# Kernel optimization log

Hardware: AMD Instinct MI355X
Metric: run time of the kernel (lower is better)

## Reference

```python
import jax, jax.numpy as jnp
import numpy as np
from jax import lax

B_, L_, C_IN = 32, 1024, 3
D_MODEL, D_STATE, D_CONV, EXPAND = 256, 16, 4, 2
D_INNER = EXPAND * D_MODEL           # 512
DT_RANK = D_MODEL // 16              # 16
N_HEADS, N_CLASS = 8, 10
LN_EPS = 1e-5


def _pos_emb(L, d):
    pos = np.arange(L, dtype=np.float32)[:, None]
    div = np.exp(np.arange(0, d, 2, dtype=np.float32) * (-np.log(10000.0) / d))
    pe = np.zeros((L, d), np.float32)
    pe[:, 0::2] = np.sin(pos * div)
    pe[:, 1::2] = np.cos(pos * div)
    return jnp.asarray(pe)


def setup_inputs() -> dict:
    key = jax.random.key(0)
    ks = jax.random.split(key, 12)
    f = lambda k, shp, s: jax.random.normal(k, shp, jnp.float32) * s
    return {
        'x_enc': f(ks[0], (B_, L_, C_IN), 1.0),
        'x_mark_enc': jnp.ones((B_, L_), jnp.float32),
        'conv_emb_w': f(ks[1], (D_MODEL, C_IN, 3), (2.0 / (C_IN * 3)) ** 0.5),
        'in_proj_w': f(ks[2], (2 * D_INNER, D_MODEL), D_MODEL ** -0.5),
        'conv1d_w': f(ks[3], (D_INNER, 1, D_CONV), D_CONV ** -0.5),
        'conv1d_b': f(ks[4], (D_INNER,), 0.02),
        'x_proj_w': f(ks[5], (DT_RANK + 2 * D_STATE, D_INNER), D_INNER ** -0.5),
        'dt_proj_w': f(ks[6], (D_INNER, DT_RANK), DT_RANK ** -0.5),
        'dt_proj_b': f(ks[7], (D_INNER,), 0.1) - 2.0,
        'A_log': jnp.log(jnp.tile(jnp.arange(1, D_STATE + 1, dtype=jnp.float32), (D_INNER, 1))),
        'D': jnp.ones((D_INNER,), jnp.float32),
        'out_proj_w': f(ks[8], (D_MODEL, D_INNER), D_INNER ** -0.5),
        'ln_g': jnp.ones((D_MODEL,), jnp.float32),
        'ln_b': jnp.zeros((D_MODEL,), jnp.float32),
        'out_w': f(ks[9], (N_CLASS, D_MODEL), D_MODEL ** -0.5),
        'attn_w': f(ks[10], (N_HEADS, D_MODEL), 0.02),
        'attn_b': jnp.ones((N_HEADS,), jnp.float32),
    }


def _forward(x_enc, x_mark_enc, conv_emb_w, in_proj_w, conv1d_w, conv1d_b,
             x_proj_w, dt_proj_w, dt_proj_b, A_log, D, out_proj_w,
             ln_g, ln_b, out_w, attn_w, attn_b):
    silu = jax.nn.silu
    # --- embedding: Conv1d 'same' with replicate padding + sinusoidal PE ---
    xp = jnp.pad(x_enc, ((0, 0), (1, 1), (0, 0)), mode='edge')      # k=3 -> pad (1,1)
    x = lax.conv_general_dilated(xp.transpose(0, 2, 1), conv_emb_w, (1,), 'VALID',
                                 dimension_numbers=('NCH', 'OIH', 'NCH')).transpose(0, 2, 1)
    x = x + _pos_emb(L_, D_MODEL)[None]                              # (B,L,D)

    # --- Mamba_TimeVariant (standard Mamba selective scan) ---
    xz = jnp.einsum('bld,ed->ble', x, in_proj_w)                     # (B,L,2*Din)
    xin, z = xz[..., :D_INNER], xz[..., D_INNER:]
    # depthwise causal conv, kernel D_CONV
    xc = jnp.pad(xin.transpose(0, 2, 1), ((0, 0), (0, 0), (D_CONV - 1, 0)))
    xc = lax.conv_general_dilated(xc, conv1d_w, (1,), 'VALID',
                                  feature_group_count=D_INNER,
                                  dimension_numbers=('NCH', 'OIH', 'NCH'))
    xc = silu(xc.transpose(0, 2, 1) + conv1d_b)                      # (B,L,Din)

    dbl = jnp.einsum('bld,ed->ble', xc, x_proj_w)                    # (B,L,dt_rank+2*N)
    dtr = dbl[..., :DT_RANK]
    Bm = dbl[..., DT_RANK:DT_RANK + D_STATE]                         # (B,L,N)
    Cm = dbl[..., DT_RANK + D_STATE:]                                # (B,L,N)
    dt = jax.nn.softplus(jnp.einsum('blr,dr->bld', dtr, dt_proj_w) + dt_proj_b)
    A = -jnp.exp(A_log)                                              # (Din,N)

    def step(h, inp):
        dt_t, B_t, C_t, x_t = inp                                    # (B,Din),(B,N),(B,N),(B,Din)
        dA = jnp.exp(dt_t[..., None] * A)                            # (B,Din,N)
        h = dA * h + dt_t[..., None] * B_t[:, None, :] * x_t[..., None]
        y = jnp.einsum('bdn,bn->bd', h, C_t)
        return h, y

    h0 = jnp.zeros((B_, D_INNER, D_STATE), xc.dtype)
    inputs = (dt.transpose(1, 0, 2), Bm.transpose(1, 0, 2),
              Cm.transpose(1, 0, 2), xc.transpose(1, 0, 2))
    _, ys = lax.scan(step, h0, inputs)                               # (L,B,Din)
    y = ys.transpose(1, 0, 2) + xc * D                               # skip via D
    y = y * silu(z)
    m = jnp.einsum('bld,ed->ble', y, out_proj_w)                     # (B,L,Dmodel)

    # LayerNorm + SiLU
    mu = m.mean(-1, keepdims=True)
    var = ((m - mu) ** 2).mean(-1, keepdims=True)
    m = (m - mu) * lax.rsqrt(var + LN_EPS) * ln_g + ln_b
    m = silu(m)

    # classification head
    logit = jnp.einsum('bld,cd->blc', m, out_w) * x_mark_enc[..., None]
    s = jnp.einsum('bld,hd->blh', m, attn_w) + attn_b                # (B,L,H)
    w = jax.nn.softmax(jnp.max(s, axis=2, keepdims=True), axis=1)    # (B,L,1)
    return (logit * w).sum(1)                                        # (B,num_class)


def reference(x_enc, x_mark_enc, conv_emb_w, in_proj_w, conv1d_w, conv1d_b,
              x_proj_w, dt_proj_w, dt_proj_b, A_log, D, out_proj_w,
              ln_g, ln_b, out_w, attn_w, attn_b):
    return _forward(x_enc, x_mark_enc, conv_emb_w, in_proj_w, conv1d_w, conv1d_b,
                    x_proj_w, dt_proj_w, dt_proj_b, A_log, D, out_proj_w,
                    ln_g, ln_b, out_w, attn_w, attn_b)
```

## Files before the change

### kernel.cpp

```cpp
#include <hip/hip_runtime.h>
#include <hip/hip_bf16.h>
#include <math.h>

#define B_  32
#define L_  1024
#define CIN 3
#define DM  256
#define DI  512
#define NST 16
#define NH  8
#define NC  10
#define M_TOT (B_*L_)

typedef unsigned short u16;
typedef __attribute__((ext_vector_type(8))) short bf16x8;
typedef __attribute__((ext_vector_type(4))) float f32x4;

static __device__ __forceinline__ float sigmoidf_(float x) {
    return 1.0f / (1.0f + __expf(-x));
}
static __device__ __forceinline__ u16 f2bf(float f) {
    unsigned int u = __float_as_uint(f);
    return (u16)((u + 0x7FFF + ((u >> 16) & 1)) >> 16);
}
static __device__ __forceinline__ float bf2f(u16 u) {
    return __uint_as_float(((unsigned int)u) << 16);
}

static __device__ __forceinline__ void reduce16_pair(float& a, float& b) {
    asm volatile(
        "s_nop 1\n\t"
        "v_add_f32 %0, %0, %0 quad_perm:[1,0,3,2] row_mask:0xf bank_mask:0xf\n\t"
        "v_add_f32 %1, %1, %1 quad_perm:[1,0,3,2] row_mask:0xf bank_mask:0xf\n\t"
        "s_nop 1\n\t"
        "v_add_f32 %0, %0, %0 quad_perm:[2,3,0,1] row_mask:0xf bank_mask:0xf\n\t"
        "v_add_f32 %1, %1, %1 quad_perm:[2,3,0,1] row_mask:0xf bank_mask:0xf\n\t"
        "s_nop 1\n\t"
        "v_add_f32 %0, %0, %0 row_ror:4 row_mask:0xf bank_mask:0xf\n\t"
        "v_add_f32 %1, %1, %1 row_ror:4 row_mask:0xf bank_mask:0xf\n\t"
        "s_nop 1\n\t"
        "v_add_f32 %0, %0, %0 row_ror:8 row_mask:0xf bank_mask:0xf\n\t"
        "v_add_f32 %1, %1, %1 row_ror:8 row_mask:0xf bank_mask:0xf\n\t"
        "s_nop 1\n\t"
        : "+v"(a), "+v"(b));
}

__global__ __launch_bounds__(256) void k_cvt(const float* __restrict__ in,
        u16* __restrict__ out) {
    int i = (blockIdx.x * 256 + threadIdx.x) * 4;
    float4 v = *(const float4*)(in + i);
    ushort4 o;
    o.x = f2bf(v.x); o.y = f2bf(v.y); o.z = f2bf(v.z); o.w = f2bf(v.w);
    *(ushort4*)(out + i) = o;
}

__global__ __launch_bounds__(256) void k_embed(const float* __restrict__ xe,
        const float* __restrict__ w, u16* __restrict__ x) {
    int bl = blockIdx.x;
    int l = bl & (L_-1);
    int b = bl >> 10;
    int d = threadIdx.x;
    const float* xb = xe + (size_t)b * L_ * CIN;
    int t0 = l > 0 ? l-1 : 0;
    int t2 = l < L_-1 ? l+1 : L_-1;
    const float* w3 = w + d*9;
    float acc = 0.f;
    #pragma unroll
    for (int i = 0; i < 3; ++i) {
        acc += xb[t0*3+i] * w3[i*3+0];
        acc += xb[l *3+i] * w3[i*3+1];
        acc += xb[t2*3+i] * w3[i*3+2];
    }
    int j = d >> 1;
    float div = expf((float)(2*j) * (-logf(10000.0f)/(float)DM));
    float ang = (float)l * div;
    acc += (d & 1) ? cosf(ang) : sinf(ang);
    x[(size_t)bl*DM + d] = f2bf(acc);
}

#define GST 40
__global__ __launch_bounds__(256) void k_gemm_mfma(
        const u16* __restrict__ A, const u16* __restrict__ W,
        float* __restrict__ O1, u16* __restrict__ O2b,
        int M, int N, int K, int S) {
    __shared__ u16 As[128*GST];
    __shared__ u16 Bs[128*GST];
    int tid = threadIdx.x;
    int row0 = blockIdx.y * 128, col0 = blockIdx.x * 128;
    int wave = tid >> 6, lane = tid & 63;
    int wr = (wave >> 1) * 64, wc = (wave & 1) * 64;
    int l16 = lane & 15, kl = lane >> 4;
    int srow = tid >> 1, skh = (tid & 1) * 16;
    const u16* Ag = A + (size_t)(row0 + srow) * K + skh;
    const u16* Wg = W + (size_t)(col0 + srow) * K + skh;

    f32x4 acc[4][4];
    #pragma unroll
    for (int m = 0; m < 4; ++m)
        #pragma unroll
        for (int n = 0; n < 4; ++n)
            acc[m][n] = (f32x4){0.f, 0.f, 0.f, 0.f};

    for (int k0 = 0; k0 < K; k0 += 32) {
        uint4 a0 = *(const uint4*)(Ag + k0);
        uint4 a1 = *(const uint4*)(Ag + k0 + 8);
        uint4 b0 = *(const uint4*)(Wg + k0);
        uint4 b1 = *(const uint4*)(Wg + k0 + 8);
        __syncthreads();
        *(uint4*)&As[srow*GST + skh]     = a0;
        *(uint4*)&As[srow*GST + skh + 8] = a1;
        *(uint4*)&Bs[srow*GST + skh]     = b0;
        *(uint4*)&Bs[srow*GST + skh + 8] = b1;
        __syncthreads();
        bf16x8 af[4], bf[4];
        #pragma unroll
        for (int m = 0; m < 4; ++m)
            af[m] = *(const bf16x8*)&As[(wr + m*16 + l16)*GST + kl*8];
        #pragma unroll
        for (int n = 0; n < 4; ++n)
            bf[n] = *(const bf16x8*)&Bs[(wc + n*16 + l16)*GST + kl*8];
        #pragma unroll
        for (int m = 0; m < 4; ++m)
            #pragma unroll
            for (int n = 0; n < 4; ++n)
                acc[m][n] = __builtin_amdgcn_mfma_f32_16x16x32_bf16(
                                af[m], bf[n], acc[m][n], 0, 0, 0);
    }

    #pragma unroll
    for (int m = 0; m < 4; ++m) {
        int rbase = row0 + wr + m*16 + kl*4;
        #pragma unroll
        for (int n = 0; n < 4; ++n) {
            int col = col0 + wc + n*16 + l16;
            #pragma unroll
            for (int r = 0; r < 4; ++r) {
                float v = acc[m][n][r];
                if (col < S) O1[(size_t)(rbase + r)*S + col] = v;
                else         O2b[(size_t)(rbase + r)*(N - S) + (col - S)] = f2bf(v);
            }
        }
    }
}

__global__ __launch_bounds__(256) void k_conv(const float* __restrict__ xin,
        const float* __restrict__ w, const float* __restrict__ bias,
        float* __restrict__ xc) {
    size_t idx = (size_t)blockIdx.x * 256 + threadIdx.x;
    int d = (int)(idx & (DI-1));
    size_t m = idx >> 9;
    int l = (int)(m & (L_-1));
    float acc = bias[d];
    #pragma unroll
    for (int k = 0; k < 4; ++k) {
        int t = l + k - 3;
        if (t >= 0)
            acc = fmaf(xin[idx + ((size_t)(k-3))*DI], w[d*4 + k], acc);
    }
    xc[idx] = acc * sigmoidf_(acc);
}

#define XBM 128
#define XBK 16
__global__ __launch_bounds__(256) void k_xproj(const float* __restrict__ xc,
        const float* __restrict__ wp, float* __restrict__ dbl) {
    __shared__ float As[XBK][XBM];
    __shared__ float Ws[XBK][48];
    int tid = threadIdx.x;
    int row0 = blockIdx.x * XBM;
    int lr = tid >> 1;
    int lk = (tid & 1) * 8;
    int we = tid >> 2;
    int wk = (tid & 3) * 4;
    int tx = tid & 15;
    int ty = tid >> 4;
    float acc[8][3];
    #pragma unroll
    for (int i = 0; i < 8; ++i)
        #pragma unroll
        for (int j = 0; j < 3; ++j) acc[i][j] = 0.f;

    for (int k0 = 0; k0 < DI; k0 += XBK) {
        float4 a0 = *(const float4*)(xc + (size_t)(row0+lr)*DI + k0 + lk);
        float4 a1 = *(const float4*)(xc + (size_t)(row0+lr)*DI + k0 + lk + 4);
        float4 w0 = make_float4(0.f,0.f,0.f,0.f);
        if (tid < 192) w0 = *(const float4*)(wp + (size_t)we*DI + k0 + wk);
        __syncthreads();
        As[lk+0][lr]=a0.x; As[lk+1][lr]=a0.y; As[lk+2][lr]=a0.z; As[lk+3][lr]=a0.w;
        As[lk+4][lr]=a1.x; As[lk+5][lr]=a1.y; As[lk+6][lr]=a1.z; As[lk+7][lr]=a1.w;
        if (tid < 192) {
            Ws[wk+0][we]=w0.x; Ws[wk+1][we]=w0.y; Ws[wk+2][we]=w0.z; Ws[wk+3][we]=w0.w;
        }
        __syncthreads();
        #pragma unroll
        for (int k = 0; k < XBK; ++k) {
            float4 av0 = *(const float4*)&As[k][ty*8];
            float4 av1 = *(const float4*)&As[k][ty*8+4];
            float w0_ = Ws[k][tx*3+0];
            float w1_ = Ws[k][tx*3+1];
            float w2_ = Ws[k][tx*3+2];
            float ar[8] = {av0.x,av0.y,av0.z,av0.w,av1.x,av1.y,av1.z,av1.w};
            #pragma unroll
            for (int i = 0; i < 8; ++i) {
                acc[i][0] = fmaf(ar[i], w0_, acc[i][0]);
                acc[i][1] = fmaf(ar[i], w1_, acc[i][1]);
                acc[i][2] = fmaf(ar[i], w2_, acc[i][2]);
            }
        }
    }
    #pragma unroll
    for (int i = 0; i < 8; ++i) {
        size_t r = row0 + ty*8 + i;
        #pragma unroll
        for (int j = 0; j < 3; ++j)
            dbl[r*48 + tx*3 + j] = acc[i][j];
    }
}

__global__ __launch_bounds__(256) void k_dtproj(const float* __restrict__ dbl,
        const float* __restrict__ dtw, const float* __restrict__ dtb,
        float* __restrict__ dt) {
    __shared__ float wl[DI][17];
    __shared__ float rl[32][16];
    size_t m0 = (size_t)blockIdx.x * 32;
    for (int i = threadIdx.x; i < DI*16; i += 256)
        wl[i >> 4][i & 15] = dtw[i];
    for (int i = threadIdx.x; i < 32*16; i += 256)
        rl[i >> 4][i & 15] = dbl[(m0 + (i>>4))*48 + (i & 15)];
    __syncthreads();
    float b0 = dtb[threadIdx.x];
    float b1 = dtb[256 + threadIdx.x];
    for (int mm = 0; mm < 32; ++mm) {
        #pragma unroll
        for (int half = 0; half < 2; ++half) {
            int d = half*256 + threadIdx.x;
            float acc = half ? b1 : b0;
            #pragma unroll
            for (int r = 0; r < 16; ++r)
                acc = fmaf(rl[mm][r], wl[d][r], acc);
            float sp = fmaxf(acc, 0.f) + log1pf(__expf(-fabsf(acc)));
            dt[(m0+mm)*DI + d] = sp;
        }
    }
}

#define SCAN_T 64
__global__ __launch_bounds__(256) void k_scan(const float* __restrict__ dt,
        const float* __restrict__ xc, const float* __restrict__ dbl,
        const float* __restrict__ A_log, const float* __restrict__ Dp,
        const u16* __restrict__ zbf, u16* __restrict__ ybf) {
    __shared__ float4 sq4[SCAN_T*17];
    __shared__ float2 sBC2[SCAN_T*17];

    int tid = threadIdx.x;
    int ch = tid >> 4;
    int n  = tid & 15;
    int d0 = blockIdx.x * 16;
    int b  = blockIdx.y;
    int d  = d0 + ch;
    float Avl2 = -expf(A_log[(size_t)d*NST + n]) * 1.44269504f;
    float h = 0.f;
    size_t base = (size_t)b * L_;

    int st = tid >> 2;
    int sc = (tid & 3) * 4;
    float4 Dv = *(const float4*)(Dp + d0 + sc);

    for (int t0 = 0; t0 < L_; t0 += SCAN_T) {
        __syncthreads();
        {
            size_t row = base + t0 + st;
            float4 dtv = *(const float4*)(dt + row*DI + d0 + sc);
            float4 xv  = *(const float4*)(xc + row*DI + d0 + sc);
            ushort4 zv4 = *(const ushort4*)(zbf + row*DI + d0 + sc);
            float4 Bv  = *(const float4*)(dbl + row*48 + 16 + sc);
            float4 Cv  = *(const float4*)(dbl + row*48 + 32 + sc);
            float z0 = bf2f(zv4.x), z1 = bf2f(zv4.y);
            float z2 = bf2f(zv4.z), z3 = bf2f(zv4.w);
            float g0 = z0 * sigmoidf_(z0);
            float g1 = z1 * sigmoidf_(z1);
            float g2 = z2 * sigmoidf_(z2);
            float g3 = z3 * sigmoidf_(z3);
            sq4[st*17 + sc+0] = make_float4(dtv.x, dtv.x*xv.x, xv.x*Dv.x*g0, g0);
            sq4[st*17 + sc+1] = make_float4(dtv.y, dtv.y*xv.y, xv.y*Dv.y*g1, g1);
            sq4[st*17 + sc+2] = make_float4(dtv.z, dtv.z*xv.z, xv.z*Dv.z*g2, g2);
            sq4[st*17 + sc+3] = make_float4(dtv.w, dtv.w*xv.w, xv.w*Dv.w*g3, g3);
            sBC2[st*17 + sc+0] = make_float2(Bv.x, Cv.x);
            sBC2[st*17 + sc+1] = make_float2(Bv.y, Cv.y);
            sBC2[st*17 + sc+2] = make_float2(Bv.z, Cv.z);
            sBC2[st*17 + sc+3] = make_float2(Bv.w, Cv.w);
        }
        __syncthreads();

        #pragma unroll 2
        for (int t2 = 0; t2 < SCAN_T/2; ++t2) {
            float2 bc0 = sBC2[(2*t2)*17 + n];
            float2 bc1 = sBC2[(2*t2+1)*17 + n];
            float4 q0 = sq4[(2*t2)*17 + ch];
            float4 q1 = sq4[(2*t2+1)*17 + ch];
            float dA = exp2f(q0.x * Avl2);
            h = fmaf(dA, h, q0.y * bc0.x);
            float p0 = h * bc0.y;
            dA = exp2f(q1.x * Avl2);
            h = fmaf(dA, h, q1.y * bc1.x);
            float p1 = h * bc1.y;
            reduce16_pair(p0, p1);
            if (n == 0) {
                size_t row = base + t0 + 2*t2;
                ybf[row*DI + d]     = f2bf(fmaf(p0, q0.w, q0.z));
                ybf[(row+1)*DI + d] = f2bf(fmaf(p1, q1.w, q1.z));
            }
        }
    }
}

__global__ __launch_bounds__(256) void k_lnsilu(float* __restrict__ m,
        const float* __restrict__ g, const float* __restrict__ bta) {
    size_t row = (size_t)blockIdx.x*4 + (threadIdx.x >> 6);
    int lane = threadIdx.x & 63;
    float4 v = *(const float4*)(m + row*DM + lane*4);
    float s = v.x + v.y + v.z + v.w;
    #pragma unroll
    for (int o = 32; o > 0; o >>= 1) s += __shfl_xor(s, o);
    float mu = s * (1.0f/DM);
    float4 c = make_float4(v.x-mu, v.y-mu, v.z-mu, v.w-mu);
    float s2 = c.x*c.x + c.y*c.y + c.z*c.z + c.w*c.w;
    #pragma unroll
    for (int o = 32; o > 0; o >>= 1) s2 += __shfl_xor(s2, o);
    float rstd = 1.0f / sqrtf(s2 * (1.0f/DM) + 1e-5f);
    float4 gv = *(const float4*)(g + lane*4);
    float4 bv = *(const float4*)(bta + lane*4);
    float o0 = c.x*rstd*gv.x + bv.x;
    float o1 = c.y*rstd*gv.y + bv.y;
    float o2 = c.z*rstd*gv.z + bv.z;
    float o3 = c.w*rstd*gv.w + bv.w;
    float4 r;
    r.x = o0 * sigmoidf_(o0);
    r.y = o1 * sigmoidf_(o1);
    r.z = o2 * sigmoidf_(o2);
    r.w = o3 * sigmoidf_(o3);
    *(float4*)(m + row*DM + lane*4) = r;
}

#define HBK 32
__global__ __launch_bounds__(256) void k_heads18(const float* __restrict__ m,
        const float* __restrict__ aw, const float* __restrict__ ow,
        float* __restrict__ r18) {
    __shared__ float As[128][36];
    __shared__ float Ws[18][36];
    int tid = threadIdx.x;
    int row0 = blockIdx.x * 128;
    int r = tid >> 1, ch = tid & 1, cb = ch * 9;
    int sr = tid >> 1, sk = (tid & 1) * 16;
    float acc[9];
    #pragma unroll
    for (int c = 0; c < 9; ++c) acc[c] = 0.f;

    for (int k0 = 0; k0 < DM; k0 += HBK) {
        float4 a[4];
        #pragma unroll
        for (int q = 0; q < 4; ++q)
            a[q] = *(const float4*)(m + (size_t)(row0+sr)*DM + k0 + sk + q*4);
        float4 wv = make_float4(0.f,0.f,0.f,0.f);
        int wc = tid >> 3, wk = (tid & 7) * 4;
        if (tid < 144) {
            const float* wsrc = (wc < NH) ? (aw + wc*DM) : (ow + (wc-NH)*DM);
            wv = *(const float4*)(wsrc + k0 + wk);
        }
        __syncthreads();
        #pragma unroll
        for (int q = 0; q < 4; ++q)
            *(float4*)&As[sr][sk + q*4] = a[q];
        if (tid < 144)
            *(float4*)&Ws[wc][wk] = wv;
        __syncthreads();
        #pragma unroll
        for (int k4 = 0; k4 < HBK/4; ++k4) {
            float4 av = *(const float4*)&As[r][k4*4];
            #pragma unroll
            for (int c = 0; c < 9; ++c) {
                float4 w4 = *(const float4*)&Ws[cb + c][k4*4];
                acc[c] += av.x*w4.x + av.y*w4.y + av.z*w4.z + av.w*w4.w;
            }
        }
        __syncthreads();
    }
    #pragma unroll
    for (int c = 0; c < 9; ++c)
        r18[(size_t)(row0 + r)*18 + cb + c] = acc[c];
}

__global__ __launch_bounds__(256) void k_final(const float* __restrict__ r18,
        const float* __restrict__ ab, const float* __restrict__ xmark,
        float* __restrict__ out) {
    __shared__ float e[L_];
    __shared__ float red[256];
    int b = blockIdx.x;
    int tid = threadIdx.x;
    float abr[NH];
    #pragma unroll
    for (int j = 0; j < NH; ++j) abr[j] = ab[j];
    float mx = -1e30f;
    for (int l = tid; l < L_; l += 256) {
        const float* rr = r18 + ((size_t)b*L_ + l)*18;
        float sm = rr[0] + abr[0];
        #pragma unroll
        for (int j = 1; j < NH; ++j) sm = fmaxf(sm, rr[j] + abr[j]);
        e[l] = sm;
        mx = fmaxf(mx, sm);
    }
    #pragma unroll
    for (int o = 32; o > 0; o >>= 1) mx = fmaxf(mx, __shfl_xor(mx, o));
    red[tid] = mx;
    __syncthreads();
    mx = fmaxf(fmaxf(red[0], red[64]), fmaxf(red[128], red[192]));
    __syncthreads();
    float ssum = 0.f;
    for (int l = tid; l < L_; l += 256) {
        float ev = __expf(e[l] - mx);
        e[l] = ev;
        ssum += ev;
    }
    #pragma unroll
    for (int o = 32; o > 0; o >>= 1) ssum += __shfl_xor(ssum, o);
    if ((tid & 63) == 0) red[tid >> 6] = ssum;
    __syncthreads();
    float inv = 1.0f / (red[0]+red[1]+red[2]+red[3]);
    float acc[NC];
    #pragma unroll
    for (int c = 0; c < NC; ++c) acc[c] = 0.f;
    for (int l = tid; l < L_; l += 256) {
        float wl = e[l] * xmark[(size_t)b*L_ + l];
        const float* lg = r18 + ((size_t)b*L_ + l)*18 + NH;
        #pragma unroll
        for (int c = 0; c < NC; ++c) acc[c] = fmaf(wl, lg[c], acc[c]);
    }
    __syncthreads();
    for (int c = 0; c < NC; ++c) {
        red[tid] = acc[c];
        __syncthreads();
        if (tid < 64) {
            float s2 = red[tid]+red[tid+64]+red[tid+128]+red[tid+192];
            #pragma unroll
            for (int o = 32; o > 0; o >>= 1) s2 += __shfl_xor(s2, o);
            if (tid == 0) out[(size_t)b*NC + c] = s2 * inv;
        }
        __syncthreads();
    }
}

extern "C" void kernel_launch(void* const* d_in, const int* in_sizes, int n_in,
                              void* d_out, int out_size, void* d_ws, size_t ws_size,
                              hipStream_t stream) {
    const float* x_enc  = (const float*)d_in[0];
    const float* x_mark = (const float*)d_in[1];
    const float* cemb_w = (const float*)d_in[2];
    const float* inp_w  = (const float*)d_in[3];
    const float* c1_w   = (const float*)d_in[4];
    const float* c1_b   = (const float*)d_in[5];
    const float* xp_w   = (const float*)d_in[6];
    const float* dtp_w  = (const float*)d_in[7];
    const float* dtp_b  = (const float*)d_in[8];
    const float* A_log  = (const float*)d_in[9];
    const float* Dp     = (const float*)d_in[10];
    const float* outp_w = (const float*)d_in[11];
    const float* ln_g   = (const float*)d_in[12];
    const float* ln_b   = (const float*)d_in[13];
    const float* out_w  = (const float*)d_in[14];
    const float* attn_w = (const float*)d_in[15];
    const float* attn_b = (const float*)d_in[16];
    float* out = (float*)d_out;

    char* ws = (char*)d_ws;
    size_t o = 0;
    u16*   xbf  = (u16*)(ws + o);  o += (size_t)M_TOT*DM*2;
    float* xin  = (float*)(ws + o); o += (size_t)M_TOT*DI*4;
    u16*   zbf  = (u16*)(ws + o);  o += (size_t)M_TOT*DI*2;
    float* xc   = (float*)(ws + o); o += (size_t)M_TOT*DI*4;
    u16*   ybf  = (u16*)(ws + o);  o += (size_t)M_TOT*DI*2;
    float* dbl  = (float*)(ws + o); o += (size_t)M_TOT*48*4;
    u16*   wbfi = (u16*)(ws + o);  o += (size_t)2*DI*DM*2;
    u16*   wbfo = (u16*)(ws + o);  o += (size_t)DM*DI*2;
    float* r18  = (float*)(ws + o); o += (size_t)M_TOT*18*4;
    float* dt = xin;
    float* mm = xc;

    k_cvt   <<<(2*DI*DM)/1024, 256, 0, stream>>>(inp_w, wbfi);
    k_cvt   <<<(DM*DI)/1024, 256, 0, stream>>>(outp_w, wbfo);
    k_embed <<<M_TOT, 256, 0, stream>>>(x_enc, cemb_w, xbf);
    k_gemm_mfma<<<dim3(8, M_TOT/128), 256, 0, stream>>>(xbf, wbfi, xin, zbf,
                                                        M_TOT, 2*DI, DM, DI);
    k_conv  <<<(M_TOT*DI)/256, 256, 0, stream>>>(xin, c1_w, c1_b, xc);
    k_xproj <<<M_TOT/XBM, 256, 0, stream>>>(xc, xp_w, dbl);
    k_dtproj<<<M_TOT/32, 256, 0, stream>>>(dbl, dtp_w, dtp_b, dt);
    k_scan  <<<dim3(DI/16, B_), 256, 0, stream>>>(dt, xc, dbl, A_log, Dp, zbf, ybf);
    k_gemm_mfma<<<dim3(2, M_TOT/128), 256, 0, stream>>>(ybf, wbfo, mm, zbf,
                                                        M_TOT, DM, DI, DM);
    k_lnsilu<<<M_TOT/4, 256, 0, stream>>>(mm, ln_g, ln_b);
    k_heads18<<<M_TOT/128, 256, 0, stream>>>(mm, attn_w, out_w, r18);
    k_final <<<B_, 256, 0, stream>>>(r18, attn_b, x_mark, out);
}
```

Measured before the change: 487.0 us.

## Vectorize depthwise conv and load scan B/C into registers with 4-step reduction

The causal depthwise conv kernel now handles four channels per thread using float4 loads and stores, cutting the thread count by four. The scan kernel no longer stages B and C through shared memory; each lane loads 16 timesteps of its state's B/C values directly into registers. It then processes four timesteps per DPP reduction, with the s_nop padding removed from the inline asm. This lowers LDS traffic and reduction overhead in the serial scan, but issues more redundant global loads of B/C across the channels in a block. Removing the s_nops relies on hardware or compiler hazard handling between dependent DPP ops.

```diff
diff --git a/kernel.cpp b/kernel.cpp
--- a/kernel.cpp
+++ b/kernel.cpp
@@ -27,22 +27,27 @@
     return __uint_as_float(((unsigned int)u) << 16);
 }
 
-static __device__ __forceinline__ void reduce16_pair(float& a, float& b) {
+static __device__ __forceinline__ void reduce16_quad(float& a, float& b,
+                                                     float& c, float& d) {
     asm volatile(
         "s_nop 1\n\t"
         "v_add_f32 %0, %0, %0 quad_perm:[1,0,3,2] row_mask:0xf bank_mask:0xf\n\t"
         "v_add_f32 %1, %1, %1 quad_perm:[1,0,3,2] row_mask:0xf bank_mask:0xf\n\t"
-        "s_nop 1\n\t"
+        "v_add_f32 %2, %2, %2 quad_perm:[1,0,3,2] row_mask:0xf bank_mask:0xf\n\t"
+        "v_add_f32 %3, %3, %3 quad_perm:[1,0,3,2] row_mask:0xf bank_mask:0xf\n\t"
         "v_add_f32 %0, %0, %0 quad_perm:[2,3,0,1] row_mask:0xf bank_mask:0xf\n\t"
         "v_add_f32 %1, %1, %1 quad_perm:[2,3,0,1] row_mask:0xf bank_mask:0xf\n\t"
-        "s_nop 1\n\t"
+        "v_add_f32 %2, %2, %2 quad_perm:[2,3,0,1] row_mask:0xf bank_mask:0xf\n\t"
+        "v_add_f32 %3, %3, %3 quad_perm:[2,3,0,1] row_mask:0xf bank_mask:0xf\n\t"
         "v_add_f32 %0, %0, %0 row_ror:4 row_mask:0xf bank_mask:0xf\n\t"
         "v_add_f32 %1, %1, %1 row_ror:4 row_mask:0xf bank_mask:0xf\n\t"
-        "s_nop 1\n\t"
+        "v_add_f32 %2, %2, %2 row_ror:4 row_mask:0xf bank_mask:0xf\n\t"
+        "v_add_f32 %3, %3, %3 row_ror:4 row_mask:0xf bank_mask:0xf\n\t"
         "v_add_f32 %0, %0, %0 row_ror:8 row_mask:0xf bank_mask:0xf\n\t"
         "v_add_f32 %1, %1, %1 row_ror:8 row_mask:0xf bank_mask:0xf\n\t"
-        "s_nop 1\n\t"
-        : "+v"(a), "+v"(b));
+        "v_add_f32 %2, %2, %2 row_ror:8 row_mask:0xf bank_mask:0xf\n\t"
+        "v_add_f32 %3, %3, %3 row_ror:8 row_mask:0xf bank_mask:0xf\n\t"
+        : "+v"(a), "+v"(b), "+v"(c), "+v"(d));
 }
 
 __global__ __launch_bounds__(256) void k_cvt(const float* __restrict__ in,
@@ -146,18 +151,34 @@
 __global__ __launch_bounds__(256) void k_conv(const float* __restrict__ xin,
         const float* __restrict__ w, const float* __restrict__ bias,
         float* __restrict__ xc) {
-    size_t idx = (size_t)blockIdx.x * 256 + threadIdx.x;
-    int d = (int)(idx & (DI-1));
-    size_t m = idx >> 9;
+    size_t i4 = (size_t)blockIdx.x * 256 + threadIdx.x;
+    int d4 = (int)(i4 & (DI/4 - 1)) * 4;
+    size_t m = i4 >> 7;
     int l = (int)(m & (L_-1));
-    float acc = bias[d];
+    float4 wv0 = *(const float4*)(w + (size_t)(d4+0)*4);
+    float4 wv1 = *(const float4*)(w + (size_t)(d4+1)*4);
+    float4 wv2 = *(const float4*)(w + (size_t)(d4+2)*4);
+    float4 wv3 = *(const float4*)(w + (size_t)(d4+3)*4);
+    float W[4][4] = {{wv0.x,wv0.y,wv0.z,wv0.w},{wv1.x,wv1.y,wv1.z,wv1.w},
+                     {wv2.x,wv2.y,wv2.z,wv2.w},{wv3.x,wv3.y,wv3.z,wv3.w}};
+    float4 acc = *(const float4*)(bias + d4);
     #pragma unroll
     for (int k = 0; k < 4; ++k) {
         int t = l + k - 3;
-        if (t >= 0)
-            acc = fmaf(xin[idx + ((size_t)(k-3))*DI], w[d*4 + k], acc);
-    }
-    xc[idx] = acc * sigmoidf_(acc);
+        if (t >= 0) {
+            float4 xv = *(const float4*)(xin + (m + k - 3)*DI + d4);
+            acc.x = fmaf(xv.x, W[0][k], acc.x);
+            acc.y = fmaf(xv.y, W[1][k], acc.y);
+            acc.z = fmaf(xv.z, W[2][k], acc.z);
+            acc.w = fmaf(xv.w, W[3][k], acc.w);
+        }
+    }
+    float4 r;
+    r.x = acc.x * sigmoidf_(acc.x);
+    r.y = acc.y * sigmoidf_(acc.y);
+    r.z = acc.z * sigmoidf_(acc.z);
+    r.w = acc.w * sigmoidf_(acc.w);
+    *(float4*)(xc + m*DI + d4) = r;
 }
 
 #define XBM 128
@@ -250,7 +271,6 @@
         const float* __restrict__ A_log, const float* __restrict__ Dp,
         const u16* __restrict__ zbf, u16* __restrict__ ybf) {
     __shared__ float4 sq4[SCAN_T*17];
-    __shared__ float2 sBC2[SCAN_T*17];
 
     int tid = threadIdx.x;
     int ch = tid >> 4;
@@ -273,8 +293,6 @@
             float4 dtv = *(const float4*)(dt + row*DI + d0 + sc);
             float4 xv  = *(const float4*)(xc + row*DI + d0 + sc);
             ushort4 zv4 = *(const ushort4*)(zbf + row*DI + d0 + sc);
-            float4 Bv  = *(const float4*)(dbl + row*48 + 16 + sc);
-            float4 Cv  = *(const float4*)(dbl + row*48 + 32 + sc);
             float z0 = bf2f(zv4.x), z1 = bf2f(zv4.y);
             float z2 = bf2f(zv4.z), z3 = bf2f(zv4.w);
             float g0 = z0 * sigmoidf_(z0);
@@ -285,30 +303,45 @@
             sq4[st*17 + sc+1] = make_float4(dtv.y, dtv.y*xv.y, xv.y*Dv.y*g1, g1);
             sq4[st*17 + sc+2] = make_float4(dtv.z, dtv.z*xv.z, xv.z*Dv.z*g2, g2);
             sq4[st*17 + sc+3] = make_float4(dtv.w, dtv.w*xv.w, xv.w*Dv.w*g3, g3);
-            sBC2[st*17 + sc+0] = make_float2(Bv.x, Cv.x);
-            sBC2[st*17 + sc+1] = make_float2(Bv.y, Cv.y);
-            sBC2[st*17 + sc+2] = make_float2(Bv.z, Cv.z);
-            sBC2[st*17 + sc+3] = make_float2(Bv.w, Cv.w);
-        }
-        __syncthreads();
-
-        #pragma unroll 2
-        for (int t2 = 0; t2 < SCAN_T/2; ++t2) {
-            float2 bc0 = sBC2[(2*t2)*17 + n];
-            float2 bc1 = sBC2[(2*t2+1)*17 + n];
-            float4 q0 = sq4[(2*t2)*17 + ch];
-            float4 q1 = sq4[(2*t2+1)*17 + ch];
-            float dA = exp2f(q0.x * Avl2);
-            h = fmaf(dA, h, q0.y * bc0.x);
-            float p0 = h * bc0.y;
-            dA = exp2f(q1.x * Avl2);
-            h = fmaf(dA, h, q1.y * bc1.x);
-            float p1 = h * bc1.y;
-            reduce16_pair(p0, p1);
-            if (n == 0) {
-                size_t row = base + t0 + 2*t2;
-                ybf[row*DI + d]     = f2bf(fmaf(p0, q0.w, q0.z));
-                ybf[(row+1)*DI + d] = f2bf(fmaf(p1, q1.w, q1.z));
+        }
+        __syncthreads();
+
+        for (int tt = 0; tt < SCAN_T; tt += 16) {
+            float Br[16], Cr[16];
+            #pragma unroll
+            for (int j = 0; j < 16; ++j) {
+                size_t r48 = (base + t0 + tt + j) * 48;
+                Br[j] = dbl[r48 + 16 + n];
+                Cr[j] = dbl[r48 + 32 + n];
+            }
+            #pragma unroll
+            for (int j4 = 0; j4 < 4; ++j4) {
+                int tb = tt + j4*4;
+                float4 q0 = sq4[(tb+0)*17 + ch];
+                float4 q1 = sq4[(tb+1)*17 + ch];
+                float4 q2 = sq4[(tb+2)*17 + ch];
+                float4 q3 = sq4[(tb+3)*17 + ch];
+                float dA;
+                dA = exp2f(q0.x * Avl2);
+                h = fmaf(dA, h, q0.y * Br[j4*4+0]);
+                float p0 = h * Cr[j4*4+0];
+                dA = exp2f(q1.x * Avl2);
+                h = fmaf(dA, h, q1.y * Br[j4*4+1]);
+                float p1 = h * Cr[j4*4+1];
+                dA = exp2f(q2.x * Avl2);
+                h = fmaf(dA, h, q2.y * Br[j4*4+2]);
+                float p2 = h * Cr[j4*4+2];
+                dA = exp2f(q3.x * Avl2);
+                h = fmaf(dA, h, q3.y * Br[j4*4+3]);
+                float p3 = h * Cr[j4*4+3];
+                reduce16_quad(p0, p1, p2, p3);
+                if (n == 0) {
+                    size_t row = base + t0 + tb;
+                    ybf[(row+0)*DI + d] = f2bf(fmaf(p0, q0.w, q0.z));
+                    ybf[(row+1)*DI + d] = f2bf(fmaf(p1, q1.w, q1.z));
+                    ybf[(row+2)*DI + d] = f2bf(fmaf(p2, q2.w, q2.z));
+                    ybf[(row+3)*DI + d] = f2bf(fmaf(p3, q3.w, q3.z));
+                }
             }
         }
     }
@@ -490,7 +523,7 @@
     k_embed <<<M_TOT, 256, 0, stream>>>(x_enc, cemb_w, xbf);
     k_gemm_mfma<<<dim3(8, M_TOT/128), 256, 0, stream>>>(xbf, wbfi, xin, zbf,
                                                         M_TOT, 2*DI, DM, DI);
-    k_conv  <<<(M_TOT*DI)/256, 256, 0, stream>>>(xin, c1_w, c1_b, xc);
+    k_conv  <<<(M_TOT*DI/4)/256, 256, 0, stream>>>(xin, c1_w, c1_b, xc);
     k_xproj <<<M_TOT/XBM, 256, 0, stream>>>(xc, xp_w, dbl);
     k_dtproj<<<M_TOT/32, 256, 0, stream>>>(dbl, dtp_w, dtp_b, dt);
     k_scan  <<<dim3(DI/16, B_), 256, 0, stream>>>(dt, xc, dbl, A_log, Dp, zbf, ybf);
```

Result: faster. 475.0 us (-2.5%).
